# Kernel tuning notes

Hardware: AMD Instinct MI355X
Metric: run time of the kernel (lower is better)

## Reference

```python
import jax, jax.numpy as jnp
import numpy as np

ATOM_FDIM = 133
BOND_FDIM = 14
DIM = 512
DEPTH = 4
N_ATOMS = 100000
N_BONDS = 300000
MAX_NB = 6
N_MOLS = 500


def _lin(x, w, b):
    return x @ w + b


def setup_inputs() -> dict:
    key = jax.random.key(0)
    ks = jax.random.split(key, 16)
    s = 0.02
    f_atoms = jax.random.normal(ks[0], (N_ATOMS, ATOM_FDIM), jnp.float32)
    f_bonds = jax.random.normal(ks[1], (N_BONDS, BOND_FDIM), jnp.float32)
    a2a = jax.random.randint(ks[2], (N_ATOMS, MAX_NB), 0, N_ATOMS, jnp.int32)
    a2b = jax.random.randint(ks[3], (N_ATOMS, MAX_NB), 0, N_BONDS, jnp.int32)
    # atom 0 is padding -> assign out-of-range segment id so segment_sum drops it
    ids = np.minimum((np.arange(N_ATOMS) - 1) // ((N_ATOMS - 1) // N_MOLS), N_MOLS - 1)
    ids[0] = N_MOLS
    mol_ids = jnp.asarray(ids, jnp.int32)
    return {
        'f_atoms': f_atoms, 'f_bonds': f_bonds, 'a2a': a2a, 'a2b': a2b,
        'mol_ids': mol_ids, 'n_mols': N_MOLS,
        'W_i_w': jax.random.normal(ks[4], (ATOM_FDIM, DIM), jnp.float32) * s,
        'W_i_b': jnp.zeros((DIM,), jnp.float32),
        'Wh0_w': jax.random.normal(ks[5], (DIM + BOND_FDIM, DIM), jnp.float32) * s,
        'Wh0_b': jnp.zeros((DIM,), jnp.float32),
        'Wh1_w': jax.random.normal(ks[6], (DIM, DIM), jnp.float32) * s,
        'Wh1_b': jnp.zeros((DIM,), jnp.float32),
        'Wh2_w': jax.random.normal(ks[7], (DIM, DIM), jnp.float32) * s,
        'Wh2_b': jnp.zeros((DIM,), jnp.float32),
        'Wah0_w': jax.random.normal(ks[8], (ATOM_FDIM, DIM), jnp.float32) * s,
        'Wah0_b': jnp.zeros((DIM,), jnp.float32),
        'Wah1_w': jax.random.normal(ks[9], (DIM, DIM), jnp.float32) * s,
        'Wah1_b': jnp.zeros((DIM,), jnp.float32),
        'Wah2_w': jax.random.normal(ks[10], (DIM, DIM), jnp.float32) * s,
        'Wah2_b': jnp.zeros((DIM,), jnp.float32),
        'W_o_w': jax.random.normal(ks[11], (2 * DIM, DIM), jnp.float32) * s,
        'W_o_b': jnp.zeros((DIM,), jnp.float32),
    }


def reference(f_atoms, f_bonds, a2a, a2b, mol_ids, n_mols,
              W_i_w, W_i_b, Wh0_w, Wh0_b, Wh1_w, Wh1_b, Wh2_w, Wh2_b,
              Wah0_w, Wah0_b, Wah1_w, Wah1_b, Wah2_w, Wah2_b, W_o_w, W_o_b):
    # input atom hidden; row 0 is padding and is zeroed
    h0 = jax.nn.relu(_lin(f_atoms, W_i_w, W_i_b))        # [A, dim]
    msg = h0.at[0].set(0.0)
    self_msg = msg
    # NOTE: original code shares one modulList across all W_h{i} -> shared weights per depth
    nei_bond_sum = jnp.sum(f_bonds[a2b], axis=1)          # [A, BOND_FDIM] (constant over depths)
    for _ in range(DEPTH):
        nei_atom_sum = jnp.sum(msg[a2a], axis=1)          # [A, dim]
        m = jnp.concatenate([nei_atom_sum, nei_bond_sum], axis=1)  # [A, dim+BOND_FDIM]
        m = _lin(jax.nn.relu(m), Wh0_w, Wh0_b)
        m = _lin(jax.nn.relu(m), Wh1_w, Wh1_b)
        m = _lin(jax.nn.relu(m), Wh2_w, Wh2_b)
        m = self_msg + m
        self_msg = m                                      # kept BEFORE zeroing row 0 (as in torch)
        msg = m.at[0].set(0.0)
    a_message = jnp.sum(msg[a2a], axis=1)                 # [A, dim]
    cc = jax.nn.relu(_lin(f_atoms, Wah0_w, Wah0_b))
    cc = jax.nn.relu(_lin(cc, Wah1_w, Wah1_b))
    cc = jax.nn.relu(_lin(cc, Wah2_w, Wah2_b))
    a_input = jnp.concatenate([cc, a_message], axis=1)    # [A, 2*dim]
    out = jax.nn.relu(_lin(a_input, W_o_w, W_o_b))        # [A, dim]
    # per-molecule sum pooling (a_scope); padding atom has id == n_mols -> dropped
    return jax.ops.segment_sum(out, mol_ids, num_segments=n_mols)
```

## Files before the change

### kernel.cpp

```cpp
#include <hip/hip_runtime.h>
#include <stdint.h>
#include <stddef.h>

typedef __attribute__((ext_vector_type(8))) _Float16 half8;
typedef __attribute__((ext_vector_type(4))) float f32x4;

__device__ __forceinline__ void gload_lds16(const void* g, void* l) {
  __builtin_amdgcn_global_load_lds(
      (const __attribute__((address_space(1))) unsigned int*)g,
      (__attribute__((address_space(3))) unsigned int*)l, 16, 0, 0);
}

__device__ __forceinline__ int sw(int row, int c) {
  return row * 64 + ((c ^ (row & 7)) << 3);
}

enum { EPI_RELU = 0, EPI_INIT = 1, EPI_DEPTH = 2 };

template <int EPI, bool SPLIT, bool ATOMS>
__global__ __launch_bounds__(256) void gemm128(
    const void* __restrict__ A1v, int lda1,
    const _Float16* __restrict__ A2, int lda2, int ksplit,
    const _Float16* __restrict__ Bt,
    const float* __restrict__ bias,
    int M, int K,
    _Float16* __restrict__ out_h, int ldo,
    const _Float16* __restrict__ self_h,
    float* self0,
    _Float16* msg_out,
    int row0)
{
  __shared__ __align__(16) _Float16 Alds[128 * 64];
  __shared__ __align__(16) _Float16 Blds[128 * 64];

  const int t = threadIdx.x;
  const int m0 = blockIdx.x * 128;
  const int n0 = blockIdx.y * 128;

  f32x4 acc[4][4];
#pragma unroll
  for (int i = 0; i < 4; ++i)
#pragma unroll
    for (int j = 0; j < 4; ++j) acc[i][j] = (f32x4){0.f, 0.f, 0.f, 0.f};

  const int lane = t & 63;
  const int w = t >> 6;
  const int wr = (w >> 1) * 64;
  const int wc = (w & 1) * 64;
  const int l16 = lane & 15;
  const int quad = lane >> 4;

  for (int kk = 0; kk < K; kk += 64) {
    __syncthreads();
#pragma unroll
    for (int h = 0; h < 4; ++h) {
      int i = t + h * 256;
      int r = i >> 3;
      int kg = (i & 7) ^ (r & 7);
      int row = m0 + r; if (row > M - 1) row = M - 1;
      int k = kk + kg * 8;
      if (ATOMS) {
        const float* src = (const float*)A1v + (size_t)row * lda1;
        half8 hv;
#pragma unroll
        for (int e = 0; e < 8; ++e) {
          int kc = k + e;
          hv[e] = (_Float16)(kc < ksplit ? src[kc] : 0.f);
        }
        *(half8*)&Alds[i * 8] = hv;
      } else {
        const _Float16* A1 = (const _Float16*)A1v;
        const _Float16* src;
        if (SPLIT) {
          src = (k < ksplit) ? (A1 + (size_t)row * lda1 + k)
                             : (A2 + (size_t)row * lda2 + (k - ksplit));
        } else {
          src = A1 + (size_t)row * lda1 + k;
        }
        gload_lds16(src, &Alds[i * 8]);
      }
    }
#pragma unroll
    for (int h = 0; h < 4; ++h) {
      int i = t + h * 256;
      int n = i >> 3;
      int kg = (i & 7) ^ (n & 7);
      gload_lds16(Bt + (size_t)(n0 + n) * K + kk + kg * 8, &Blds[i * 8]);
    }
    __syncthreads();

    half8 af[4][2], bf[4][2];
#pragma unroll
    for (int kh = 0; kh < 2; ++kh) {
#pragma unroll
      for (int mi = 0; mi < 4; ++mi)
        af[mi][kh] = *(const half8*)&Alds[sw(wr + mi * 16 + l16, kh * 4 + quad)];
#pragma unroll
      for (int ni = 0; ni < 4; ++ni)
        bf[ni][kh] = *(const half8*)&Blds[sw(wc + ni * 16 + l16, kh * 4 + quad)];
    }
#pragma unroll
    for (int kh = 0; kh < 2; ++kh)
#pragma unroll
      for (int mi = 0; mi < 4; ++mi)
#pragma unroll
        for (int ni = 0; ni < 4; ++ni)
          acc[mi][ni] = __builtin_amdgcn_mfma_f32_16x16x32_f16(
              af[mi][kh], bf[ni][kh], acc[mi][ni], 0, 0, 0);
  }

#pragma unroll
  for (int mi = 0; mi < 4; ++mi) {
#pragma unroll
    for (int ni = 0; ni < 4; ++ni) {
      int col = n0 + wc + ni * 16 + l16;
      float b = bias[col];
#pragma unroll
      for (int r = 0; r < 4; ++r) {
        int row = m0 + wr + mi * 16 + quad * 4 + r;
        if (row < M) {
          float v = acc[mi][ni][r] + b;
          if (EPI == EPI_RELU) {
            v = fmaxf(v, 0.f);
            out_h[(size_t)row * ldo + col] = (_Float16)v;
          } else if (EPI == EPI_INIT) {
            v = fmaxf(v, 0.f);
            if (row == row0) { msg_out[(size_t)row * 512 + col] = (_Float16)0.f; self0[col] = 0.f; }
            else msg_out[(size_t)row * 512 + col] = (_Float16)v;
          } else {
            float self = (row == row0) ? self0[col]
                                       : (float)self_h[(size_t)row * 512 + col];
            v += self;
            if (row == row0) { self0[col] = v; msg_out[(size_t)row * 512 + col] = (_Float16)0.f; }
            else msg_out[(size_t)row * 512 + col] = (_Float16)v;
          }
        }
      }
    }
  }
}

template <bool SPLIT>
__global__ __launch_bounds__(256) void gemm_wide(
    const _Float16* __restrict__ A1, int lda1,
    const _Float16* __restrict__ A2, int lda2, int ksplit,
    const _Float16* __restrict__ Bt, const float* __restrict__ bias,
    int M, int K,
    _Float16* __restrict__ out_h)
{
  __shared__ __align__(16) _Float16 Alds[64 * 32];
  __shared__ __align__(16) _Float16 Blds[512 * 32];
  const int t = threadIdx.x;
  const int m0 = blockIdx.x * 64;
  f32x4 acc[4][8];
#pragma unroll
  for (int i = 0; i < 4; ++i)
#pragma unroll
    for (int j = 0; j < 8; ++j) acc[i][j] = (f32x4){0.f, 0.f, 0.f, 0.f};
  const int lane = t & 63;
  const int w = t >> 6;
  const int wc = w * 128;
  const int l16 = lane & 15;
  const int quad = lane >> 4;
  for (int kk = 0; kk < K; kk += 32) {
    __syncthreads();
    {
      int r = t >> 2, kg = t & 3;
      int row = m0 + r; if (row > M - 1) row = M - 1;
      int k = kk + kg * 8;
      const _Float16* src;
      if (SPLIT) {
        src = (k < ksplit) ? (A1 + (size_t)row * lda1 + k)
                           : (A2 + (size_t)row * lda2 + (k - ksplit));
      } else {
        src = A1 + (size_t)row * lda1 + k;
      }
      gload_lds16(src, &Alds[t * 8]);
    }
#pragma unroll
    for (int h = 0; h < 8; ++h) {
      int i = t + h * 256;
      int n = i >> 2, kg = i & 3;
      gload_lds16(Bt + (size_t)n * K + kk + kg * 8, &Blds[i * 8]);
    }
    __syncthreads();
    half8 af[4], bf[8];
#pragma unroll
    for (int mi = 0; mi < 4; ++mi)
      af[mi] = *(const half8*)&Alds[(mi * 16 + l16) * 32 + quad * 8];
#pragma unroll
    for (int ni = 0; ni < 8; ++ni)
      bf[ni] = *(const half8*)&Blds[(wc + ni * 16 + l16) * 32 + quad * 8];
#pragma unroll
    for (int mi = 0; mi < 4; ++mi)
#pragma unroll
      for (int ni = 0; ni < 8; ++ni)
        acc[mi][ni] = __builtin_amdgcn_mfma_f32_16x16x32_f16(af[mi], bf[ni], acc[mi][ni], 0, 0, 0);
  }
#pragma unroll
  for (int mi = 0; mi < 4; ++mi) {
#pragma unroll
    for (int ni = 0; ni < 8; ++ni) {
      int col = wc + ni * 16 + l16;
      float b = bias[col];
#pragma unroll
      for (int r = 0; r < 4; ++r) {
        int row = m0 + mi * 16 + quad * 4 + r;
        if (row < M) {
          float v = fmaxf(acc[mi][ni][r] + b, 0.f);
          out_h[(size_t)row * 512 + col] = (_Float16)v;
        }
      }
    }
  }
}

template <bool RELU>
__global__ __launch_bounds__(256) void gather_k(
    const _Float16* __restrict__ msg, const int* __restrict__ a2a,
    _Float16* __restrict__ out, int rows)
{
  int t = threadIdx.x;
  int a = blockIdx.x * 4 + (t >> 6);
  if (a >= rows) return;
  int g = t & 63;
  const _Float16* base = msg + g * 8;
  float acc[8] = {0, 0, 0, 0, 0, 0, 0, 0};
#pragma unroll
  for (int j = 0; j < 6; ++j) {
    int nb = a2a[(size_t)a * 6 + j];
    half8 v = *(const half8*)(base + (size_t)nb * 512);
#pragma unroll
    for (int e = 0; e < 8; ++e) acc[e] += (float)v[e];
  }
  half8 o;
#pragma unroll
  for (int e = 0; e < 8; ++e) {
    float x = acc[e];
    if (RELU) x = fmaxf(x, 0.f);
    o[e] = (_Float16)x;
  }
  *(half8*)(out + (size_t)a * 512 + g * 8) = o;
}

__global__ __launch_bounds__(256) void bondsum_k(
    const float* __restrict__ fb, const int* __restrict__ a2b,
    _Float16* __restrict__ bnd, int A)
{
  int idx = blockIdx.x * 256 + threadIdx.x;
  int a = idx >> 6, c = idx & 63;
  if (a >= A) return;
  float s = 0.f;
  if (c < 14) {
#pragma unroll
    for (int j = 0; j < 6; ++j) s += fb[(size_t)a2b[a * 6 + j] * 14 + c];
    s = fmaxf(s, 0.f);
  }
  bnd[(size_t)a * 64 + c] = (_Float16)s;
}

__global__ __launch_bounds__(256) void padatoms_k(
    const float* __restrict__ fa, _Float16* __restrict__ ap, int A)
{
  int idx = blockIdx.x * 256 + threadIdx.x;
  if (idx >= A * 24) return;
  int a = idx / 24, c8 = (idx - a * 24) * 8;
  const float* src = fa + (size_t)a * 133;
  half8 hv;
#pragma unroll
  for (int e = 0; e < 8; ++e) {
    int c = c8 + e;
    hv[e] = (_Float16)(c < 133 ? src[c] : 0.f);
  }
  *(half8*)(ap + (size_t)a * 192 + c8) = hv;
}

struct WJobs {
  const float* src[8];
  _Float16* dst[8];
  int K[8];
  int Kpad[8];
};
__global__ __launch_bounds__(256) void wcast_all(WJobs j) {
  int job = blockIdx.y;
  int idx = blockIdx.x * 256 + threadIdx.x;
  int Kpad = j.Kpad[job];
  if (idx >= 512 * Kpad) return;
  int n = idx / Kpad, k = idx - n * Kpad;
  float v = (k < j.K[job]) ? j.src[job][(size_t)k * 512 + n] : 0.f;
  j.dst[job][idx] = (_Float16)v;
}

__global__ __launch_bounds__(256) void fill_k(float* __restrict__ p, int n, float v) {
  int i = blockIdx.x * 256 + threadIdx.x;
  if (i < n) p[i] = v;
}

__global__ __launch_bounds__(256) void segsum_k(
    const _Float16* __restrict__ x, const int* __restrict__ mol,
    float* __restrict__ out, int A, int n_mols)
{
  int t = threadIdx.x;
  int c = t * 2;
  int a0 = blockIdx.x * 128;
  int aend = a0 + 128; if (aend > A) aend = A;
  float s0 = 0.f, s1 = 0.f;
  int cur = -1;
  for (int a = a0; a < aend; ++a) {
    int m = mol[a];
    if (m != cur) {
      if (cur >= 0 && cur < n_mols) {
        atomicAdd(&out[(size_t)cur * 512 + c], s0);
        atomicAdd(&out[(size_t)cur * 512 + c + 1], s1);
      }
      cur = m; s0 = 0.f; s1 = 0.f;
    }
    const _Float16* row = x + (size_t)a * 512 + c;
    s0 += (float)row[0];
    s1 += (float)row[1];
  }
  if (cur >= 0 && cur < n_mols) {
    atomicAdd(&out[(size_t)cur * 512 + c], s0);
    atomicAdd(&out[(size_t)cur * 512 + c + 1], s1);
  }
}

extern "C" void kernel_launch(void* const* d_in, const int* in_sizes, int n_in,
                              void* d_out, int out_size, void* d_ws, size_t ws_size,
                              hipStream_t stream) {
  const float* f_atoms = (const float*)d_in[0];
  const float* f_bonds = (const float*)d_in[1];
  const int* a2a = (const int*)d_in[2];
  const int* a2b = (const int*)d_in[3];
  const int* mol_ids = (const int*)d_in[4];
  const float* W_i_w  = (const float*)d_in[6];
  const float* W_i_b  = (const float*)d_in[7];
  const float* Wh0_w  = (const float*)d_in[8];
  const float* Wh0_b  = (const float*)d_in[9];
  const float* Wh1_w  = (const float*)d_in[10];
  const float* Wh1_b  = (const float*)d_in[11];
  const float* Wh2_w  = (const float*)d_in[12];
  const float* Wh2_b  = (const float*)d_in[13];
  const float* Wah0_w = (const float*)d_in[14];
  const float* Wah0_b = (const float*)d_in[15];
  const float* Wah1_w = (const float*)d_in[16];
  const float* Wah1_b = (const float*)d_in[17];
  const float* Wah2_w = (const float*)d_in[18];
  const float* Wah2_b = (const float*)d_in[19];
  const float* W_o_w  = (const float*)d_in[20];
  const float* W_o_b  = (const float*)d_in[21];

  const int A = in_sizes[0] / 133;
  const int n_mols = out_size / 512;

  char* ws = (char*)d_ws;
  size_t off = 0;
  auto alloc = [&](size_t bytes) -> void* {
    void* p = ws + off;
    off = (off + bytes + 255) & ~(size_t)255;
    return p;
  };
  const size_t big = (size_t)A * 512 * 2;
  _Float16* MSGA = (_Float16*)alloc(big);
  _Float16* MSGB = (_Float16*)alloc(big);
  _Float16* BND = (_Float16*)alloc((size_t)A * 64 * 2);
  _Float16* Wt_i   = (_Float16*)alloc(512 * 192 * 2);
  _Float16* Wt_h0  = (_Float16*)alloc(512 * 576 * 2);
  _Float16* Wt_h1  = (_Float16*)alloc(512 * 512 * 2);
  _Float16* Wt_h2  = (_Float16*)alloc(512 * 512 * 2);
  _Float16* Wt_ah0 = (_Float16*)alloc(512 * 192 * 2);
  _Float16* Wt_ah1 = (_Float16*)alloc(512 * 512 * 2);
  _Float16* Wt_ah2 = (_Float16*)alloc(512 * 512 * 2);
  _Float16* Wt_o   = (_Float16*)alloc(512 * 1024 * 2);
  float* SELF0 = (float*)alloc(512 * 4);
  const size_t fixed = off;

  if (ws_size < fixed) {
    fill_k<<<(out_size + 255) / 256, 256, 0, stream>>>(
        (float*)d_out, out_size, (float)(ws_size >> 20));
    return;
  }

  const size_t scratch = ws_size - fixed;
  const size_t apbytes = (size_t)A * 192 * 2;
  const bool useAp = scratch >= apbytes + 256;
  _Float16* Ap = (_Float16*)(ws + fixed);

  int crows = (int)(scratch / 2 / 1024);
  crows &= ~127;
  const int Acap = (A + 127) & ~127;
  if (crows > Acap) crows = Acap;
  const bool chunked = crows >= 2048;

  {
    WJobs j;
    j.src[0] = W_i_w;  j.dst[0] = Wt_i;   j.K[0] = 133;  j.Kpad[0] = 192;
    j.src[1] = Wh0_w;  j.dst[1] = Wt_h0;  j.K[1] = 526;  j.Kpad[1] = 576;
    j.src[2] = Wh1_w;  j.dst[2] = Wt_h1;  j.K[2] = 512;  j.Kpad[2] = 512;
    j.src[3] = Wh2_w;  j.dst[3] = Wt_h2;  j.K[3] = 512;  j.Kpad[3] = 512;
    j.src[4] = Wah0_w; j.dst[4] = Wt_ah0; j.K[4] = 133;  j.Kpad[4] = 192;
    j.src[5] = Wah1_w; j.dst[5] = Wt_ah1; j.K[5] = 512;  j.Kpad[5] = 512;
    j.src[6] = Wah2_w; j.dst[6] = Wt_ah2; j.K[6] = 512;  j.Kpad[6] = 512;
    j.src[7] = W_o_w;  j.dst[7] = Wt_o;   j.K[7] = 1024; j.Kpad[7] = 1024;
    dim3 g((512 * 1024 + 255) / 256, 8);
    wcast_all<<<g, 256, 0, stream>>>(j);
  }
  bondsum_k<<<((A * 64) + 255) / 256, 256, 0, stream>>>(f_bonds, a2b, BND, A);

  dim3 gfull((A + 127) / 128, 4);

  if (useAp) {
    padatoms_k<<<((A * 24) + 255) / 256, 256, 0, stream>>>(f_atoms, Ap, A);
    gemm128<EPI_INIT, false, false><<<gfull, 256, 0, stream>>>(
        Ap, 192, nullptr, 0, 0, Wt_i, W_i_b, A, 192,
        nullptr, 0, nullptr, SELF0, MSGA, 0);
  } else {
    gemm128<EPI_INIT, false, true><<<gfull, 256, 0, stream>>>(
        f_atoms, 133, nullptr, 0, 133, Wt_i, W_i_b, A, 192,
        nullptr, 0, nullptr, SELF0, MSGA, 0);
  }

  if (chunked) {
    _Float16* YC = (_Float16*)(ws + fixed);
    _Float16* NC = (_Float16*)(ws + fixed + (size_t)crows * 1024);
    _Float16* MO = MSGA;
    _Float16* MN = MSGB;
    for (int d = 0; d < 4; ++d) {
      gather_k<true><<<(A + 3) / 4, 256, 0, stream>>>(MO, a2a, MN, A);
      for (int r0 = 0; r0 < A; r0 += crows) {
        int rows = A - r0 < crows ? A - r0 : crows;
        dim3 gg((rows + 127) / 128, 4);
        int row0 = (r0 == 0) ? 0 : -1;
        gemm128<EPI_RELU, true, false><<<gg, 256, 0, stream>>>(
            MN + (size_t)r0 * 512, 512, BND + (size_t)r0 * 64, 64, 512,
            Wt_h0, Wh0_b, rows, 576, YC, 512, nullptr, nullptr, nullptr, 0);
        gemm128<EPI_RELU, false, false><<<gg, 256, 0, stream>>>(
            YC, 512, nullptr, 0, 0, Wt_h1, Wh1_b, rows, 512,
            NC, 512, nullptr, nullptr, nullptr, 0);
        gemm128<EPI_DEPTH, false, false><<<gg, 256, 0, stream>>>(
            NC, 512, nullptr, 0, 0, Wt_h2, Wh2_b, rows, 512,
            nullptr, 0, MO + (size_t)r0 * 512, SELF0, MN + (size_t)r0 * 512, row0);
      }
      _Float16* tmp = MO; MO = MN; MN = tmp;
    }
    gather_k<false><<<(A + 3) / 4, 256, 0, stream>>>(MO, a2a, MN, A);
    if (useAp) {
      padatoms_k<<<((A * 24) + 255) / 256, 256, 0, stream>>>(f_atoms, Ap, A);
      gemm128<EPI_RELU, false, false><<<gfull, 256, 0, stream>>>(
          Ap, 192, nullptr, 0, 0, Wt_ah0, Wah0_b, A, 192,
          MO, 512, nullptr, nullptr, nullptr, 0);
    } else {
      gemm128<EPI_RELU, false, true><<<gfull, 256, 0, stream>>>(
          f_atoms, 133, nullptr, 0, 133, Wt_ah0, Wah0_b, A, 192,
          MO, 512, nullptr, nullptr, nullptr, 0);
    }
    for (int r0 = 0; r0 < A; r0 += crows) {
      int rows = A - r0 < crows ? A - r0 : crows;
      dim3 gg((rows + 127) / 128, 4);
      gemm128<EPI_RELU, false, false><<<gg, 256, 0, stream>>>(
          MO + (size_t)r0 * 512, 512, nullptr, 0, 0, Wt_ah1, Wah1_b, rows, 512,
          YC, 512, nullptr, nullptr, nullptr, 0);
      gemm128<EPI_RELU, false, false><<<gg, 256, 0, stream>>>(
          YC, 512, nullptr, 0, 0, Wt_ah2, Wah2_b, rows, 512,
          NC, 512, nullptr, nullptr, nullptr, 0);
      gemm128<EPI_RELU, true, false><<<gg, 256, 0, stream>>>(
          NC, 512, MN + (size_t)r0 * 512, 512, 512, Wt_o, W_o_b, rows, 1024,
          MO + (size_t)r0 * 512, 512, nullptr, nullptr, nullptr, 0);
    }
    fill_k<<<(out_size + 255) / 256, 256, 0, stream>>>((float*)d_out, out_size, 0.f);
    segsum_k<<<(A + 127) / 128, 256, 0, stream>>>(MO, mol_ids, (float*)d_out, A, n_mols);
  } else {
    _Float16* MSG = MSGA;
    _Float16* Y1b = MSGB;
    const int gw = (A + 63) / 64;
    const int gg = (A + 3) / 4;
    for (int d = 0; d < 4; ++d) {
      gather_k<true><<<gg, 256, 0, stream>>>(MSG, a2a, Y1b, A);
      gemm_wide<true><<<gw, 256, 0, stream>>>(
          Y1b, 512, BND, 64, 512, Wt_h0, Wh0_b, A, 576, Y1b);
      gemm_wide<false><<<gw, 256, 0, stream>>>(
          Y1b, 512, nullptr, 0, 0, Wt_h1, Wh1_b, A, 512, Y1b);
      gemm128<EPI_DEPTH, false, false><<<gfull, 256, 0, stream>>>(
          Y1b, 512, nullptr, 0, 0, Wt_h2, Wh2_b, A, 512,
          nullptr, 0, MSG, SELF0, MSG, 0);
    }
    gather_k<false><<<gg, 256, 0, stream>>>(MSG, a2a, Y1b, A);
    gemm128<EPI_RELU, false, true><<<gfull, 256, 0, stream>>>(
        f_atoms, 133, nullptr, 0, 133, Wt_ah0, Wah0_b, A, 192,
        MSG, 512, nullptr, nullptr, nullptr, 0);
    gemm_wide<false><<<gw, 256, 0, stream>>>(
        MSG, 512, nullptr, 0, 0, Wt_ah1, Wah1_b, A, 512, MSG);
    gemm_wide<false><<<gw, 256, 0, stream>>>(
        MSG, 512, nullptr, 0, 0, Wt_ah2, Wah2_b, A, 512, MSG);
    gemm_wide<true><<<gw, 256, 0, stream>>>(
        MSG, 512, Y1b, 512, 512, Wt_o, W_o_b, A, 1024, Y1b);
    fill_k<<<(out_size + 255) / 256, 256, 0, stream>>>((float*)d_out, out_size, 0.f);
    segsum_k<<<(A + 127) / 128, 256, 0, stream>>>(Y1b, mol_ids, (float*)d_out, A, n_mols);
  }
}
```

Before: 3.371 ms.

## Fuse neighbor gather-sum into GEMM A-tile loads in chunked path

Removes the standalone gather kernels in the chunked path. The 6-neighbor message sum (with ReLU for the Wh0 layer) is now computed directly while loading A tiles in the Wh0 and W_o GEMMs, and buffer roles are reshuffled to match. This avoids writing and re-reading a full [A,512] gathered buffer each depth. In exchange, every output-column block (4 per row tile) redoes the 6-way random gather, and the gather goes through registers instead of async LDS loads.

```diff
diff --git a/kernel.cpp b/kernel.cpp
--- a/kernel.cpp
+++ b/kernel.cpp
@@ -17,10 +17,12 @@
 
 enum { EPI_RELU = 0, EPI_INIT = 1, EPI_DEPTH = 2 };
 
-template <int EPI, bool SPLIT, bool ATOMS>
+template <int EPI, bool SPLIT, bool ATOMS, bool GA1, bool GA2, bool GRELU>
 __global__ __launch_bounds__(256) void gemm128(
     const void* __restrict__ A1v, int lda1,
     const _Float16* __restrict__ A2, int lda2, int ksplit,
+    const _Float16* __restrict__ gmsg,
+    const int* __restrict__ a2a_loc,
     const _Float16* __restrict__ Bt,
     const float* __restrict__ bias,
     int M, int K,
@@ -59,25 +61,47 @@
       int kg = (i & 7) ^ (r & 7);
       int row = m0 + r; if (row > M - 1) row = M - 1;
       int k = kk + kg * 8;
-      if (ATOMS) {
-        const float* src = (const float*)A1v + (size_t)row * lda1;
-        half8 hv;
-#pragma unroll
-        for (int e = 0; e < 8; ++e) {
-          int kc = k + e;
-          hv[e] = (_Float16)(kc < ksplit ? src[kc] : 0.f);
+      bool seg1 = !SPLIT || (k < ksplit);
+      if (seg1) {
+        if (ATOMS) {
+          const float* src = (const float*)A1v + (size_t)row * lda1;
+          half8 hv;
+#pragma unroll
+          for (int e = 0; e < 8; ++e) {
+            int kc = k + e;
+            hv[e] = (_Float16)(kc < ksplit ? src[kc] : 0.f);
+          }
+          *(half8*)&Alds[i * 8] = hv;
+        } else if (GA1) {
+          const int* nb = a2a_loc + (size_t)row * 6;
+          half8 s = {};
+#pragma unroll
+          for (int j = 0; j < 6; ++j) {
+            half8 v = *(const half8*)(gmsg + (size_t)nb[j] * 512 + k);
+            s += v;
+          }
+          if (GRELU) {
+#pragma unroll
+            for (int e = 0; e < 8; ++e) s[e] = (s[e] < (_Float16)0.f) ? (_Float16)0.f : s[e];
+          }
+          *(half8*)&Alds[i * 8] = s;
+        } else {
+          gload_lds16((const _Float16*)A1v + (size_t)row * lda1 + k, &Alds[i * 8]);
         }
-        *(half8*)&Alds[i * 8] = hv;
       } else {
-        const _Float16* A1 = (const _Float16*)A1v;
-        const _Float16* src;
-        if (SPLIT) {
-          src = (k < ksplit) ? (A1 + (size_t)row * lda1 + k)
-                             : (A2 + (size_t)row * lda2 + (k - ksplit));
+        if (GA2) {
+          int c = k - ksplit;
+          const int* nb = a2a_loc + (size_t)row * 6;
+          half8 s = {};
+#pragma unroll
+          for (int j = 0; j < 6; ++j) {
+            half8 v = *(const half8*)(gmsg + (size_t)nb[j] * 512 + c);
+            s += v;
+          }
+          *(half8*)&Alds[i * 8] = s;
         } else {
-          src = A1 + (size_t)row * lda1 + k;
+          gload_lds16(A2 + (size_t)row * lda2 + (k - ksplit), &Alds[i * 8]);
         }
-        gload_lds16(src, &Alds[i * 8]);
       }
     }
 #pragma unroll
@@ -411,12 +435,12 @@
 
   if (useAp) {
     padatoms_k<<<((A * 24) + 255) / 256, 256, 0, stream>>>(f_atoms, Ap, A);
-    gemm128<EPI_INIT, false, false><<<gfull, 256, 0, stream>>>(
-        Ap, 192, nullptr, 0, 0, Wt_i, W_i_b, A, 192,
+    gemm128<EPI_INIT, false, false, false, false, false><<<gfull, 256, 0, stream>>>(
+        Ap, 192, nullptr, 0, 0, nullptr, nullptr, Wt_i, W_i_b, A, 192,
         nullptr, 0, nullptr, SELF0, MSGA, 0);
   } else {
-    gemm128<EPI_INIT, false, true><<<gfull, 256, 0, stream>>>(
-        f_atoms, 133, nullptr, 0, 133, Wt_i, W_i_b, A, 192,
+    gemm128<EPI_INIT, false, true, false, false, false><<<gfull, 256, 0, stream>>>(
+        f_atoms, 133, nullptr, 0, 133, nullptr, nullptr, Wt_i, W_i_b, A, 192,
         nullptr, 0, nullptr, SELF0, MSGA, 0);
   }
 
@@ -426,49 +450,49 @@
     _Float16* MO = MSGA;
     _Float16* MN = MSGB;
     for (int d = 0; d < 4; ++d) {
-      gather_k<true><<<(A + 3) / 4, 256, 0, stream>>>(MO, a2a, MN, A);
       for (int r0 = 0; r0 < A; r0 += crows) {
         int rows = A - r0 < crows ? A - r0 : crows;
         dim3 gg((rows + 127) / 128, 4);
         int row0 = (r0 == 0) ? 0 : -1;
-        gemm128<EPI_RELU, true, false><<<gg, 256, 0, stream>>>(
-            MN + (size_t)r0 * 512, 512, BND + (size_t)r0 * 64, 64, 512,
-            Wt_h0, Wh0_b, rows, 576, YC, 512, nullptr, nullptr, nullptr, 0);
-        gemm128<EPI_RELU, false, false><<<gg, 256, 0, stream>>>(
-            YC, 512, nullptr, 0, 0, Wt_h1, Wh1_b, rows, 512,
+        gemm128<EPI_RELU, true, false, true, false, true><<<gg, 256, 0, stream>>>(
+            nullptr, 0, BND + (size_t)r0 * 64, 64, 512,
+            MO, a2a + (size_t)r0 * 6, Wt_h0, Wh0_b, rows, 576,
+            YC, 512, nullptr, nullptr, nullptr, 0);
+        gemm128<EPI_RELU, false, false, false, false, false><<<gg, 256, 0, stream>>>(
+            YC, 512, nullptr, 0, 0, nullptr, nullptr, Wt_h1, Wh1_b, rows, 512,
             NC, 512, nullptr, nullptr, nullptr, 0);
-        gemm128<EPI_DEPTH, false, false><<<gg, 256, 0, stream>>>(
-            NC, 512, nullptr, 0, 0, Wt_h2, Wh2_b, rows, 512,
+        gemm128<EPI_DEPTH, false, false, false, false, false><<<gg, 256, 0, stream>>>(
+            NC, 512, nullptr, 0, 0, nullptr, nullptr, Wt_h2, Wh2_b, rows, 512,
             nullptr, 0, MO + (size_t)r0 * 512, SELF0, MN + (size_t)r0 * 512, row0);
       }
       _Float16* tmp = MO; MO = MN; MN = tmp;
     }
-    gather_k<false><<<(A + 3) / 4, 256, 0, stream>>>(MO, a2a, MN, A);
     if (useAp) {
       padatoms_k<<<((A * 24) + 255) / 256, 256, 0, stream>>>(f_atoms, Ap, A);
-      gemm128<EPI_RELU, false, false><<<gfull, 256, 0, stream>>>(
-          Ap, 192, nullptr, 0, 0, Wt_ah0, Wah0_b, A, 192,
-          MO, 512, nullptr, nullptr, nullptr, 0);
+      gemm128<EPI_RELU, false, false, false, false, false><<<gfull, 256, 0, stream>>>(
+          Ap, 192, nullptr, 0, 0, nullptr, nullptr, Wt_ah0, Wah0_b, A, 192,
+          MN, 512, nullptr, nullptr, nullptr, 0);
     } else {
-      gemm128<EPI_RELU, false, true><<<gfull, 256, 0, stream>>>(
-          f_atoms, 133, nullptr, 0, 133, Wt_ah0, Wah0_b, A, 192,
-          MO, 512, nullptr, nullptr, nullptr, 0);
+      gemm128<EPI_RELU, false, true, false, false, false><<<gfull, 256, 0, stream>>>(
+          f_atoms, 133, nullptr, 0, 133, nullptr, nullptr, Wt_ah0, Wah0_b, A, 192,
+          MN, 512, nullptr, nullptr, nullptr, 0);
     }
     for (int r0 = 0; r0 < A; r0 += crows) {
       int rows = A - r0 < crows ? A - r0 : crows;
       dim3 gg((rows + 127) / 128, 4);
-      gemm128<EPI_RELU, false, false><<<gg, 256, 0, stream>>>(
-          MO + (size_t)r0 * 512, 512, nullptr, 0, 0, Wt_ah1, Wah1_b, rows, 512,
-          YC, 512, nullptr, nullptr, nullptr, 0);
-      gemm128<EPI_RELU, false, false><<<gg, 256, 0, stream>>>(
-          YC, 512, nullptr, 0, 0, Wt_ah2, Wah2_b, rows, 512,
-          NC, 512, nullptr, nullptr, nullptr, 0);
-      gemm128<EPI_RELU, true, false><<<gg, 256, 0, stream>>>(
-          NC, 512, MN + (size_t)r0 * 512, 512, 512, Wt_o, W_o_b, rows, 1024,
-          MO + (size_t)r0 * 512, 512, nullptr, nullptr, nullptr, 0);
+      gemm128<EPI_RELU, false, false, false, false, false><<<gg, 256, 0, stream>>>(
+          MN + (size_t)r0 * 512, 512, nullptr, 0, 0, nullptr, nullptr,
+          Wt_ah1, Wah1_b, rows, 512, YC, 512, nullptr, nullptr, nullptr, 0);
+      gemm128<EPI_RELU, false, false, false, false, false><<<gg, 256, 0, stream>>>(
+          YC, 512, nullptr, 0, 0, nullptr, nullptr,
+          Wt_ah2, Wah2_b, rows, 512, NC, 512, nullptr, nullptr, nullptr, 0);
+      gemm128<EPI_RELU, true, false, false, true, false><<<gg, 256, 0, stream>>>(
+          NC, 512, nullptr, 0, 512,
+          MO, a2a + (size_t)r0 * 6, Wt_o, W_o_b, rows, 1024,
+          MN + (size_t)r0 * 512, 512, nullptr, nullptr, nullptr, 0);
     }
     fill_k<<<(out_size + 255) / 256, 256, 0, stream>>>((float*)d_out, out_size, 0.f);
-    segsum_k<<<(A + 127) / 128, 256, 0, stream>>>(MO, mol_ids, (float*)d_out, A, n_mols);
+    segsum_k<<<(A + 127) / 128, 256, 0, stream>>>(MN, mol_ids, (float*)d_out, A, n_mols);
   } else {
     _Float16* MSG = MSGA;
     _Float16* Y1b = MSGB;
@@ -480,13 +504,13 @@
           Y1b, 512, BND, 64, 512, Wt_h0, Wh0_b, A, 576, Y1b);
       gemm_wide<false><<<gw, 256, 0, stream>>>(
           Y1b, 512, nullptr, 0, 0, Wt_h1, Wh1_b, A, 512, Y1b);
-      gemm128<EPI_DEPTH, false, false><<<gfull, 256, 0, stream>>>(
-          Y1b, 512, nullptr, 0, 0, Wt_h2, Wh2_b, A, 512,
+      gemm128<EPI_DEPTH, false, false, false, false, false><<<gfull, 256, 0, stream>>>(
+          Y1b, 512, nullptr, 0, 0, nullptr, nullptr, Wt_h2, Wh2_b, A, 512,
           nullptr, 0, MSG, SELF0, MSG, 0);
     }
     gather_k<false><<<gg, 256, 0, stream>>>(MSG, a2a, Y1b, A);
-    gemm128<EPI_RELU, false, true><<<gfull, 256, 0, stream>>>(
-        f_atoms, 133, nullptr, 0, 133, Wt_ah0, Wah0_b, A, 192,
+    gemm128<EPI_RELU, false, true, false, false, false><<<gfull, 256, 0, stream>>>(
+        f_atoms, 133, nullptr, 0, 133, nullptr, nullptr, Wt_ah0, Wah0_b, A, 192,
         MSG, 512, nullptr, nullptr, nullptr, 0);
     gemm_wide<false><<<gw, 256, 0, stream>>>(
         MSG, 512, nullptr, 0, 0, Wt_ah1, Wah1_b, A, 512, MSG);
```

Measured after the change: 3.767 ms. 1.12x slower.
